# Performance work log

Hardware: AMD Instinct MI355X
Metric: run time of the kernel (lower is better)

Reference implementation:

```python
import jax, jax.numpy as jnp
import numpy as np

S = 7
B = 2
NUM_CLASS = 16
LAMBDA_LOC = 10.0
LAMBDA_NOOBJ = 0.5


def _corners(box):
    # box: [M, >=4] -> lt/rb corners per original scaling (center*64 +/- size*224)
    cx = box[:, 0] * 64.0
    cy = box[:, 1] * 64.0
    hw = box[:, 2] * 224.0
    hh = box[:, 3] * 224.0
    return cx - hw, cy - hh, cx + hw, cy + hh


def _iou(b1, b2):
    l1, t1, r1, bo1 = _corners(b1)
    l2, t2, r2, bo2 = _corners(b2)
    xA = jnp.maximum(l1, l2)
    yA = jnp.maximum(t1, t2)
    xB = jnp.minimum(r1, r2)
    yB = jnp.minimum(bo1, bo2)
    inter = jnp.maximum(0.0, xB - xA + 1.0) * jnp.maximum(0.0, yB - yA + 1.0)
    a1 = (r1 - l1 + 1.0) * (bo1 - t1 + 1.0)
    a2 = (r2 - l2 + 1.0) * (bo2 - t2 + 1.0)
    return inter / (a1 + a2 - inter)


def setup_inputs() -> dict:
    key = jax.random.key(0)
    k1, k2, k3 = jax.random.split(key, 3)
    N = 16384
    predict = jax.random.uniform(k1, (N, S, S, 5 * B + NUM_CLASS), dtype=jnp.float32)
    target = jax.random.uniform(k2, (N, S, S, 5 * B + NUM_CLASS), dtype=jnp.float32)
    conf = (jax.random.uniform(k3, (N, S, S, 1)) < 0.3).astype(jnp.float32)
    target = target.at[..., 4:5].set(conf).at[..., 9:10].set(conf)
    return {"predict": predict, "target": target}


def reference(predict, target):
    C = 5 * B + NUM_CLASS
    p = predict.reshape(-1, C)  # [M, 26], M = N*49
    t = target.reshape(-1, C)

    obj = t[:, 4]              # 0/1 objectness mask per grid cell
    noobj = 1.0 - obj

    tbox = t[:, :4]
    iou1 = _iou(p[:, :4], tbox)
    iou2 = _iou(p[:, 5:9], tbox)
    best2 = iou2 > iou1        # argmax with tie -> box1, matching torch argmax
    iou_max = jnp.where(best2, iou2, iou1)

    vp = jnp.where(best2[:, None], p[:, 5:10], p[:, :5])   # responsible pred box
    vt_xywh = jnp.where(best2[:, None], t[:, 5:9], t[:, :4])

    xy_loss = jnp.sum(obj * jnp.sum((vp[:, :2] - vt_xywh[:, :2]) ** 2, axis=1))
    wh_loss = jnp.sum(obj * jnp.sum((jnp.sqrt(vp[:, 2:4]) - jnp.sqrt(vt_xywh[:, 2:4])) ** 2, axis=1))
    obj_conf_loss = jnp.sum(obj * (vp[:, 4] - iou_max) ** 2)

    noobj_conf1 = jnp.sum(noobj * (p[:, 4] - t[:, 4]) ** 2)
    noobj_conf2 = jnp.sum(noobj * (p[:, 9] - t[:, 9]) ** 2)

    class_loss = jnp.sum(obj * jnp.sum((p[:, 10:] - t[:, 10:]) ** 2, axis=1))

    total = (LAMBDA_LOC * xy_loss + LAMBDA_LOC * wh_loss + obj_conf_loss
             + LAMBDA_NOOBJ * (noobj_conf1 + noobj_conf2) + 2.0 * class_loss)
    return total
```

## Files before the change

### kernel.cpp

```cpp
#include <hip/hip_runtime.h>

constexpr int C = 26;
constexpr int TILE_ROWS = 128;
constexpr int THREADS = 256;
constexpr int TILE_FLOATS = TILE_ROWS * C;
constexpr float LAMBDA_LOC = 10.0f;
constexpr float LAMBDA_NOOBJ = 0.5f;

__device__ __forceinline__ void stage16(const float* g, float* lds_uniform) {
    __builtin_amdgcn_global_load_lds(
        (const __attribute__((address_space(1))) unsigned int*)g,
        (__attribute__((address_space(3))) unsigned int*)lds_uniform,
        16, 0, 0);
}

__device__ __forceinline__ float iou_f(float b1x, float b1y, float b1w, float b1h,
                                       float b2x, float b2y, float b2w, float b2h) {
    float cx1 = b1x * 64.f, cy1 = b1y * 64.f, hw1 = b1w * 224.f, hh1 = b1h * 224.f;
    float l1 = cx1 - hw1, t1 = cy1 - hh1, r1 = cx1 + hw1, bo1 = cy1 + hh1;
    float cx2 = b2x * 64.f, cy2 = b2y * 64.f, hw2 = b2w * 224.f, hh2 = b2h * 224.f;
    float l2 = cx2 - hw2, t2 = cy2 - hh2, r2 = cx2 + hw2, bo2 = cy2 + hh2;
    float xA = fmaxf(l1, l2), yA = fmaxf(t1, t2);
    float xB = fminf(r1, r2), yB = fminf(bo1, bo2);
    float iw = fmaxf(0.f, xB - xA + 1.f);
    float ih = fmaxf(0.f, yB - yA + 1.f);
    float inter = iw * ih;
    float a1 = (r1 - l1 + 1.f) * (bo1 - t1 + 1.f);
    float a2 = (r2 - l2 + 1.f) * (bo2 - t2 + 1.f);
    return inter / (a1 + a2 - inter);
}

__global__ __launch_bounds__(THREADS, 6) void yolo_main(
    const float* __restrict__ pred, const float* __restrict__ targ,
    float* __restrict__ partial)
{
    __shared__ float lds_p[TILE_FLOATS];
    __shared__ float lds_t[TILE_FLOATS];

    const int tid  = threadIdx.x;
    const int wid  = tid >> 6;
    const size_t tile_base = (size_t)blockIdx.x * TILE_FLOATS;
    const float* ptile = pred + tile_base;
    const float* ttile = targ + tile_base;

    #pragma unroll
    for (int k = 0; k < 3; ++k) {
        int j = k * 256 + tid;
        int u = (k * 256 + wid * 64) * 4;
        stage16(ptile + j * 4, lds_p + u);
        stage16(ttile + j * 4, lds_t + u);
    }
    if (wid == 0) {
        int j = 3 * 256 + tid;
        int u = (3 * 256) * 4;
        stage16(ptile + j * 4, lds_p + u);
        stage16(ttile + j * 4, lds_t + u);
    }
    __syncthreads();

    float acc = 0.f;
    if (tid < TILE_ROWS) {
        const float2* pr = reinterpret_cast<const float2*>(lds_p + tid * C);
        const float2* tr = reinterpret_cast<const float2*>(lds_t + tid * C);

        float2 p01 = pr[0], p23 = pr[1], p45 = pr[2], p67 = pr[3], p89 = pr[4];
        float2 t01 = tr[0], t23 = tr[1], t45 = tr[2], t67 = tr[3], t89 = tr[4];

        float cls = 0.f;
        #pragma unroll
        for (int j = 5; j < 13; ++j) {
            float2 a = pr[j], b = tr[j];
            float dx = a.x - b.x, dy = a.y - b.y;
            cls = fmaf(dx, dx, cls);
            cls = fmaf(dy, dy, cls);
        }

        float obj   = t45.x;
        float noobj = 1.f - obj;

        float iou1 = iou_f(p01.x, p01.y, p23.x, p23.y, t01.x, t01.y, t23.x, t23.y);
        float iou2 = iou_f(p45.y, p67.x, p67.y, p89.x, t01.x, t01.y, t23.x, t23.y);

        bool  best2 = iou2 > iou1;
        float iou_m = best2 ? iou2 : iou1;

        float vpx = best2 ? p45.y : p01.x;
        float vpy = best2 ? p67.x : p01.y;
        float vpw = best2 ? p67.y : p23.x;
        float vph = best2 ? p89.x : p23.y;
        float vpc = best2 ? p89.y : p45.x;
        float vtx = best2 ? t45.y : t01.x;
        float vty = best2 ? t67.x : t01.y;
        float vtw = best2 ? t67.y : t23.x;
        float vth = best2 ? t89.x : t23.y;

        float dx = vpx - vtx, dy = vpy - vty;
        float xy = dx * dx + dy * dy;
        float sw = sqrtf(vpw) - sqrtf(vtw);
        float sh = sqrtf(vph) - sqrtf(vth);
        float wh = sw * sw + sh * sh;
        float dc = vpc - iou_m;
        float oc = dc * dc;
        float d1 = p45.x - t45.x;
        float d2 = p89.y - t89.y;

        acc = obj * (LAMBDA_LOC * (xy + wh) + oc + 2.f * cls)
            + LAMBDA_NOOBJ * noobj * (d1 * d1 + d2 * d2);
    }

    #pragma unroll
    for (int off = 32; off > 0; off >>= 1)
        acc += __shfl_down(acc, off);

    __shared__ float wsum[THREADS / 64];
    int lane = tid & 63;
    if (lane == 0) wsum[wid] = acc;
    __syncthreads();
    if (tid == 0) {
        float s = 0.f;
        #pragma unroll
        for (int w = 0; w < THREADS / 64; ++w) s += wsum[w];
        partial[blockIdx.x] = s;
    }
}

__global__ __launch_bounds__(1024) void yolo_reduce(
    const float* __restrict__ partial, float* __restrict__ out, int n)
{
    float acc = 0.f;
    for (int i = threadIdx.x; i < n; i += 1024) acc += partial[i];
    #pragma unroll
    for (int off = 32; off > 0; off >>= 1)
        acc += __shfl_down(acc, off);
    __shared__ float wsum[16];
    int lane = threadIdx.x & 63, wid = threadIdx.x >> 6;
    if (lane == 0) wsum[wid] = acc;
    __syncthreads();
    if (threadIdx.x == 0) {
        float s = 0.f;
        #pragma unroll
        for (int w = 0; w < 16; ++w) s += wsum[w];
        out[0] = s;
    }
}

extern "C" void kernel_launch(void* const* d_in, const int* in_sizes, int n_in,
                              void* d_out, int out_size, void* d_ws, size_t ws_size,
                              hipStream_t stream) {
    const float* pred = (const float*)d_in[0];
    const float* targ = (const float*)d_in[1];
    float* out = (float*)d_out;
    float* partial = (float*)d_ws;
    int rows = in_sizes[0] / C;
    int n_tiles = rows / TILE_ROWS;

    yolo_main<<<n_tiles, THREADS, 0, stream>>>(pred, targ, partial);
    yolo_reduce<<<1, 1024, 0, stream>>>(partial, out, n_tiles);
}
```

Measured before the change: 33.14 us.

## Use persistent double-buffered blocks and atomic final reduction instead of second kernel

Launches a fixed grid of 768 persistent blocks, each looping over tiles. While computing the current tile, each block prefetches the next tile into a second LDS buffer with global_load_lds. The separate reduce kernel is replaced by a memset plus one atomicAdd per block, which removes a kernel launch. The risks are extra LDS per block (occupancy lowered to 3), a nondeterministic float summation order, and an extra memset dispatch.

```diff
diff --git a/kernel.cpp b/kernel.cpp
--- a/kernel.cpp
+++ b/kernel.cpp
@@ -3,6 +3,7 @@
 constexpr int C = 26;
 constexpr int TILE_ROWS = 128;
 constexpr int THREADS = 256;
+constexpr int GRID = 768;
 constexpr int TILE_FLOATS = TILE_ROWS * C;
 constexpr float LAMBDA_LOC = 10.0f;
 constexpr float LAMBDA_NOOBJ = 0.5f;
@@ -12,6 +13,22 @@
         (const __attribute__((address_space(1))) unsigned int*)g,
         (__attribute__((address_space(3))) unsigned int*)lds_uniform,
         16, 0, 0);
+}
+
+__device__ __forceinline__ void stage_tile(const float* gp, const float* gt,
+                                           float* lp, float* lt, int tid, int wid) {
+    #pragma unroll
+    for (int k = 0; k < 3; ++k) {
+        int j = k * 256 + tid;
+        int u = (k * 256 + wid * 64) * 4;
+        stage16(gp + j * 4, lp + u);
+        stage16(gt + j * 4, lt + u);
+    }
+    if (wid == 0) {
+        int j = 768 + tid;
+        stage16(gp + j * 4, lp + 768 * 4);
+        stage16(gt + j * 4, lt + 768 * 4);
+    }
 }
 
 __device__ __forceinline__ float iou_f(float b1x, float b1y, float b1w, float b1h,
@@ -30,82 +47,82 @@
     return inter / (a1 + a2 - inter);
 }
 
-__global__ __launch_bounds__(THREADS, 6) void yolo_main(
+__device__ __forceinline__ float row_loss(const float* lds_p, const float* lds_t, int row) {
+    const float2* pr = reinterpret_cast<const float2*>(lds_p + row * C);
+    const float2* tr = reinterpret_cast<const float2*>(lds_t + row * C);
+
+    float2 p01 = pr[0], p23 = pr[1], p45 = pr[2], p67 = pr[3], p89 = pr[4];
+    float2 t01 = tr[0], t23 = tr[1], t45 = tr[2], t67 = tr[3], t89 = tr[4];
+
+    float cls = 0.f;
+    #pragma unroll
+    for (int j = 5; j < 13; ++j) {
+        float2 a = pr[j], b = tr[j];
+        float dx = a.x - b.x, dy = a.y - b.y;
+        cls = fmaf(dx, dx, cls);
+        cls = fmaf(dy, dy, cls);
+    }
+
+    float obj   = t45.x;
+    float noobj = 1.f - obj;
+
+    float iou1 = iou_f(p01.x, p01.y, p23.x, p23.y, t01.x, t01.y, t23.x, t23.y);
+    float iou2 = iou_f(p45.y, p67.x, p67.y, p89.x, t01.x, t01.y, t23.x, t23.y);
+
+    bool  best2 = iou2 > iou1;
+    float iou_m = best2 ? iou2 : iou1;
+
+    float vpx = best2 ? p45.y : p01.x;
+    float vpy = best2 ? p67.x : p01.y;
+    float vpw = best2 ? p67.y : p23.x;
+    float vph = best2 ? p89.x : p23.y;
+    float vpc = best2 ? p89.y : p45.x;
+    float vtx = best2 ? t45.y : t01.x;
+    float vty = best2 ? t67.x : t01.y;
+    float vtw = best2 ? t67.y : t23.x;
+    float vth = best2 ? t89.x : t23.y;
+
+    float dx = vpx - vtx, dy = vpy - vty;
+    float xy = dx * dx + dy * dy;
+    float sw = sqrtf(vpw) - sqrtf(vtw);
+    float sh = sqrtf(vph) - sqrtf(vth);
+    float wh = sw * sw + sh * sh;
+    float dc = vpc - iou_m;
+    float oc = dc * dc;
+    float d1 = p45.x - t45.x;
+    float d2 = p89.y - t89.y;
+
+    return obj * (LAMBDA_LOC * (xy + wh) + oc + 2.f * cls)
+         + LAMBDA_NOOBJ * noobj * (d1 * d1 + d2 * d2);
+}
+
+__global__ __launch_bounds__(THREADS, 3) void yolo_main(
     const float* __restrict__ pred, const float* __restrict__ targ,
-    float* __restrict__ partial)
+    float* __restrict__ out, int nTiles)
 {
-    __shared__ float lds_p[TILE_FLOATS];
-    __shared__ float lds_t[TILE_FLOATS];
+    __shared__ float lp[2][TILE_FLOATS];
+    __shared__ float lt[2][TILE_FLOATS];
 
-    const int tid  = threadIdx.x;
-    const int wid  = tid >> 6;
-    const size_t tile_base = (size_t)blockIdx.x * TILE_FLOATS;
-    const float* ptile = pred + tile_base;
-    const float* ttile = targ + tile_base;
+    const int tid = threadIdx.x;
+    const int wid = tid >> 6;
+    float acc = 0.f;
 
-    #pragma unroll
-    for (int k = 0; k < 3; ++k) {
-        int j = k * 256 + tid;
-        int u = (k * 256 + wid * 64) * 4;
-        stage16(ptile + j * 4, lds_p + u);
-        stage16(ttile + j * 4, lds_t + u);
-    }
-    if (wid == 0) {
-        int j = 3 * 256 + tid;
-        int u = (3 * 256) * 4;
-        stage16(ptile + j * 4, lds_p + u);
-        stage16(ttile + j * 4, lds_t + u);
-    }
+    int t = blockIdx.x;
+    if (t < nTiles)
+        stage_tile(pred + (size_t)t * TILE_FLOATS, targ + (size_t)t * TILE_FLOATS,
+                   lp[0], lt[0], tid, wid);
     __syncthreads();
 
-    float acc = 0.f;
-    if (tid < TILE_ROWS) {
-        const float2* pr = reinterpret_cast<const float2*>(lds_p + tid * C);
-        const float2* tr = reinterpret_cast<const float2*>(lds_t + tid * C);
-
-        float2 p01 = pr[0], p23 = pr[1], p45 = pr[2], p67 = pr[3], p89 = pr[4];
-        float2 t01 = tr[0], t23 = tr[1], t45 = tr[2], t67 = tr[3], t89 = tr[4];
-
-        float cls = 0.f;
-        #pragma unroll
-        for (int j = 5; j < 13; ++j) {
-            float2 a = pr[j], b = tr[j];
-            float dx = a.x - b.x, dy = a.y - b.y;
-            cls = fmaf(dx, dx, cls);
-            cls = fmaf(dy, dy, cls);
-        }
-
-        float obj   = t45.x;
-        float noobj = 1.f - obj;
-
-        float iou1 = iou_f(p01.x, p01.y, p23.x, p23.y, t01.x, t01.y, t23.x, t23.y);
-        float iou2 = iou_f(p45.y, p67.x, p67.y, p89.x, t01.x, t01.y, t23.x, t23.y);
-
-        bool  best2 = iou2 > iou1;
-        float iou_m = best2 ? iou2 : iou1;
-
-        float vpx = best2 ? p45.y : p01.x;
-        float vpy = best2 ? p67.x : p01.y;
-        float vpw = best2 ? p67.y : p23.x;
-        float vph = best2 ? p89.x : p23.y;
-        float vpc = best2 ? p89.y : p45.x;
-        float vtx = best2 ? t45.y : t01.x;
-        float vty = best2 ? t67.x : t01.y;
-        float vtw = best2 ? t67.y : t23.x;
-        float vth = best2 ? t89.x : t23.y;
-
-        float dx = vpx - vtx, dy = vpy - vty;
-        float xy = dx * dx + dy * dy;
-        float sw = sqrtf(vpw) - sqrtf(vtw);
-        float sh = sqrtf(vph) - sqrtf(vth);
-        float wh = sw * sw + sh * sh;
-        float dc = vpc - iou_m;
-        float oc = dc * dc;
-        float d1 = p45.x - t45.x;
-        float d2 = p89.y - t89.y;
-
-        acc = obj * (LAMBDA_LOC * (xy + wh) + oc + 2.f * cls)
-            + LAMBDA_NOOBJ * noobj * (d1 * d1 + d2 * d2);
+    int cur = 0;
+    for (; t < nTiles; t += GRID) {
+        int tn = t + GRID;
+        if (tn < nTiles)
+            stage_tile(pred + (size_t)tn * TILE_FLOATS, targ + (size_t)tn * TILE_FLOATS,
+                       lp[cur ^ 1], lt[cur ^ 1], tid, wid);
+        if (tid < TILE_ROWS)
+            acc += row_loss(lp[cur], lt[cur], tid);
+        __syncthreads();
+        cur ^= 1;
     }
 
     #pragma unroll
@@ -113,35 +130,10 @@
         acc += __shfl_down(acc, off);
 
     __shared__ float wsum[THREADS / 64];
-    int lane = tid & 63;
-    if (lane == 0) wsum[wid] = acc;
+    if ((tid & 63) == 0) wsum[wid] = acc;
     __syncthreads();
-    if (tid == 0) {
-        float s = 0.f;
-        #pragma unroll
-        for (int w = 0; w < THREADS / 64; ++w) s += wsum[w];
-        partial[blockIdx.x] = s;
-    }
-}
-
-__global__ __launch_bounds__(1024) void yolo_reduce(
-    const float* __restrict__ partial, float* __restrict__ out, int n)
-{
-    float acc = 0.f;
-    for (int i = threadIdx.x; i < n; i += 1024) acc += partial[i];
-    #pragma unroll
-    for (int off = 32; off > 0; off >>= 1)
-        acc += __shfl_down(acc, off);
-    __shared__ float wsum[16];
-    int lane = threadIdx.x & 63, wid = threadIdx.x >> 6;
-    if (lane == 0) wsum[wid] = acc;
-    __syncthreads();
-    if (threadIdx.x == 0) {
-        float s = 0.f;
-        #pragma unroll
-        for (int w = 0; w < 16; ++w) s += wsum[w];
-        out[0] = s;
-    }
+    if (tid == 0)
+        atomicAdd(out, wsum[0] + wsum[1] + wsum[2] + wsum[3]);
 }
 
 extern "C" void kernel_launch(void* const* d_in, const int* in_sizes, int n_in,
@@ -150,10 +142,9 @@
     const float* pred = (const float*)d_in[0];
     const float* targ = (const float*)d_in[1];
     float* out = (float*)d_out;
-    float* partial = (float*)d_ws;
     int rows = in_sizes[0] / C;
-    int n_tiles = rows / TILE_ROWS;
+    int nTiles = rows / TILE_ROWS;
 
-    yolo_main<<<n_tiles, THREADS, 0, stream>>>(pred, targ, partial);
-    yolo_reduce<<<1, 1024, 0, stream>>>(partial, out, n_tiles);
+    hipMemsetAsync(out, 0, sizeof(float), stream);
+    yolo_main<<<GRID, THREADS, 0, stream>>>(pred, targ, out, nTiles);
 }
```

Result: slower. 40.62 us (+22.6%).
